# Kernel tuning notes

Measured on AMD Instinct MI355X. Metric: run time of the kernel, lower is better.

The kernel has to match this reference:

```python
import jax, jax.numpy as jnp
import numpy as np

VOCAB = 50257
EMB = 1024
HID = 1024
B, T = 8, 256


def setup_inputs() -> dict:
    key = jax.random.key(0)
    ks = jax.random.split(key, 6)
    s = 0.05  # small init scale for numerical sanity
    return {
        "x": jax.random.randint(ks[0], (B, T), 0, VOCAB, dtype=jnp.int64) if jax.config.jax_enable_x64 else jax.random.randint(ks[0], (B, T), 0, VOCAB, dtype=jnp.int32),
        "emb_W": jax.random.normal(ks[1], (VOCAB, EMB), dtype=jnp.float32) * s,
        "W_ih": jax.random.normal(ks[2], (4 * HID, EMB), dtype=jnp.float32) * s,
        "W_hh": jax.random.normal(ks[3], (4 * HID, HID), dtype=jnp.float32) * s,
        "b_ih": jax.random.normal(ks[4], (4 * HID,), dtype=jnp.float32) * s,
        "b_hh": jax.random.normal(ks[5], (4 * HID,), dtype=jnp.float32) * s,
        "dec_b": jnp.zeros((VOCAB,), dtype=jnp.float32),
    }


def _lstm(emb, W_ih, W_hh, b_ih, b_hh):
    # emb: [B, T, E]. Precompute input projections for all timesteps (one big GEMM).
    x_proj = jnp.einsum("bte,ge->btg", emb, W_ih) + (b_ih + b_hh)  # [B, T, 4H]
    h0 = jnp.zeros((emb.shape[0], HID), emb.dtype)
    c0 = jnp.zeros((emb.shape[0], HID), emb.dtype)

    def step(carry, xt):  # xt: [B, 4H]
        h, c = carry
        g = xt + h @ W_hh.T  # [B, 4H]
        i, f, gg, o = jnp.split(g, 4, axis=-1)  # PyTorch gate order i,f,g,o
        i = jax.nn.sigmoid(i)
        f = jax.nn.sigmoid(f)
        gg = jnp.tanh(gg)
        o = jax.nn.sigmoid(o)
        c_new = f * c + i * gg
        h_new = o * jnp.tanh(c_new)
        return (h_new, c_new), h_new

    (hT, cT), hs = jax.lax.scan(step, (h0, c0), jnp.swapaxes(x_proj, 0, 1))
    out = jnp.swapaxes(hs, 0, 1)  # [B, T, H], batch_first
    return out, (hT[None], cT[None])  # num_layers=1 leading dim


def reference(x, emb_W, W_ih, W_hh, b_ih, b_hh, dec_b):
    emb = emb_W[x]                                   # [B, T, E]
    out, hidden = _lstm(emb, W_ih, W_hh, b_ih, b_hh)  # [B, T, H]
    logits = jnp.einsum("bth,vh->btv", out, emb_W) + dec_b  # tied decoder
    logits = logits.reshape(-1, VOCAB)
    return jax.nn.log_softmax(logits, axis=1), hidden
```

## Files before the change

### kernel.cpp

```cpp
#include <hip/hip_runtime.h>

typedef float f32x4 __attribute__((ext_vector_type(4)));
typedef __bf16 bf16x8 __attribute__((ext_vector_type(8)));
typedef unsigned short u16;
typedef unsigned int u32;

#define VOCAB 50257
#define KDIM 1024
#define MROWS 2048
#define TSEQ 256
#define NBLK 64
#define LOGN ((size_t)MROWS * VOCAB)

__device__ __forceinline__ u16 f2bf(float f) {
    u32 u = __builtin_bit_cast(u32, f);
    u = (u + 0x7FFFu + ((u >> 16) & 1u)) >> 16;
    return (u16)u;
}

__device__ __forceinline__ float sigm(float x) { return 1.0f / (1.0f + __expf(-x)); }


__global__ void conv_bf16(const float4* __restrict__ in, ushort4* __restrict__ out, long n4) {
    long i = (long)blockIdx.x * blockDim.x + threadIdx.x;
    long stride = (long)gridDim.x * blockDim.x;
    for (; i < n4; i += stride) {
        float4 v = in[i];
        ushort4 o;
        o.x = f2bf(v.x); o.y = f2bf(v.y); o.z = f2bf(v.z); o.w = f2bf(v.w);
        out[i] = o;
    }
}

__global__ void bias_sum(const float* __restrict__ a, const float* __restrict__ b,
                         float* __restrict__ o) {
    int i = blockIdx.x * 256 + threadIdx.x;
    if (i < 4096) o[i] = a[i] + b[i];
}

__global__ __launch_bounds__(256) void gather_emb(const int* __restrict__ x,
                                                  const float* __restrict__ embW,
                                                  u16* __restrict__ out) {
    int m = blockIdx.x;
    int row = x[m];
    const float4* src = (const float4*)(embW + (size_t)row * KDIM);
    ushort4* dst = (ushort4*)(out + (size_t)m * KDIM);
    float4 v = src[threadIdx.x];
    ushort4 o;
    o.x = f2bf(v.x); o.y = f2bf(v.y); o.z = f2bf(v.z); o.w = f2bf(v.w);
    dst[threadIdx.x] = o;
}


#define BM 128
#define BN 128
#define BK 64

__device__ __forceinline__ void gl_lds16(const u16* g, const u16* l) {
    __builtin_amdgcn_global_load_lds(
        (const __attribute__((address_space(1))) u32*)g,
        (__attribute__((address_space(3))) u32*)l, 16, 0, 0);
}

__global__ __launch_bounds__(256, 2)
void gemm_bt(const u16* __restrict__ A, const u16* __restrict__ Bm,
             const float* __restrict__ bias, float* __restrict__ C,
             int N, int Nb, int K, int ldc)
{
    __shared__ __align__(16) u16 As[BM * BK];
    __shared__ __align__(16) u16 Bs[BN * BK];
    const int tid  = threadIdx.x;
    const int lane = tid & 63;
    const int wid  = tid >> 6;

    const int gx  = gridDim.x;
    const int nwg = gx * gridDim.y;
    const int lin = blockIdx.y * gx + blockIdx.x;
    const int qq = nwg >> 3, rr = nwg & 7;
    const int xcd = lin & 7, idx = lin >> 3;
    const int neu = (xcd < rr) ? (xcd * (qq + 1) + idx)
                               : (rr * (qq + 1) + (xcd - rr) * qq + idx);
    const int bm = neu % gx;
    const int bn = neu / gx;

    const int wr = wid >> 1, wc = wid & 1;

    const u16* gA[4]; const u16* gB[4];
    const u16* ldsA[4]; const u16* ldsB[4];
#pragma unroll
    for (int r = 0; r < 4; ++r) {
        int L = r * 256 + tid;
        int row = L >> 3, ps = L & 7;
        int ls = ps ^ (row & 7);
        gA[r] = A + (size_t)(bm * BM + row) * K + ls * 8;
        int brow = bn * BN + row; brow = brow < Nb ? brow : Nb - 1;
        gB[r] = Bm + (size_t)brow * K + ls * 8;
        ldsA[r] = As + (r * 256 + wid * 64) * 8;
        ldsB[r] = Bs + (r * 256 + wid * 64) * 8;
    }

    const int lrow = lane & 15, ksl = lane >> 4;
    int aoff[4][2], boff[4][2];
#pragma unroll
    for (int i = 0; i < 4; ++i)
#pragma unroll
        for (int ks = 0; ks < 2; ++ks) {
            int ar = wr * 64 + i * 16 + lrow;
            aoff[i][ks] = ar * BK + (((ks * 4 + ksl) ^ (ar & 7)) * 8);
            int br = wc * 64 + i * 16 + lrow;
            boff[i][ks] = br * BK + (((ks * 4 + ksl) ^ (br & 7)) * 8);
        }

    f32x4 acc[4][4] = {};
    for (int kt = 0; kt < K; kt += BK) {
#pragma unroll
        for (int r = 0; r < 4; ++r) gl_lds16(gA[r] + kt, ldsA[r]);
#pragma unroll
        for (int r = 0; r < 4; ++r) gl_lds16(gB[r] + kt, ldsB[r]);
        __syncthreads();
        bf16x8 af[4][2], bfb[4][2];
#pragma unroll
        for (int i = 0; i < 4; ++i)
#pragma unroll
            for (int ks = 0; ks < 2; ++ks) {
                af[i][ks]  = *(const bf16x8*)(As + aoff[i][ks]);
                bfb[i][ks] = *(const bf16x8*)(Bs + boff[i][ks]);
            }
#pragma unroll
        for (int ks = 0; ks < 2; ++ks)
#pragma unroll
            for (int mi = 0; mi < 4; ++mi)
#pragma unroll
                for (int ni = 0; ni < 4; ++ni)
                    acc[mi][ni] = __builtin_amdgcn_mfma_f32_16x16x32_bf16(
                        af[mi][ks], bfb[ni][ks], acc[mi][ni], 0, 0, 0);
        __syncthreads();
    }

    const int crl = lane >> 4, ccl = lane & 15;
    const int row0 = bm * BM + wr * 64, col0 = bn * BN + wc * 64;
#pragma unroll
    for (int ni = 0; ni < 4; ++ni) {
        int col = col0 + ni * 16 + ccl;
        if (col < N) {
            float bv = bias[col];
#pragma unroll
            for (int mi = 0; mi < 4; ++mi) {
                int row = row0 + mi * 16 + crl * 4;
                float* cp = C + (size_t)row * ldc + col;
#pragma unroll
                for (int r = 0; r < 4; ++r)
                    cp[(size_t)r * ldc] = acc[mi][ni][r] + bv;
            }
        }
    }
}


__global__ __launch_bounds__(256, 1)
void lstm_persist(const u16* __restrict__ Whh,
                  const float* __restrict__ xproj,
                  u16* __restrict__ hbuf2,
                  u16* __restrict__ hall,
                  float* __restrict__ outTail,
                  u32* __restrict__ flags)
{
    const int tid  = threadIdx.x;
    const int lane = tid & 63;
    const int wq   = tid >> 6;
    const int lrow = lane & 15, ksl = lane >> 4;
    const int bid  = blockIdx.x;
    const int colbase = bid * 16;

    bf16x8 Bf[32];
    {
        const u16* bp = Whh + (size_t)(wq * 1024 + colbase + lrow) * KDIM + ksl * 8;
#pragma unroll
        for (int kk = 0; kk < 32; ++kk)
            asm volatile("global_load_dwordx4 %0, %1, off"
                         : "=v"(Bf[kk]) : "v"(bp + kk * 32));
        asm volatile("s_waitcnt vmcnt(0)" ::: "memory");
        __builtin_amdgcn_sched_barrier(0);
    }

    __shared__ float S[4][8][16];

    const bool upd = tid < 128;
    const int b8 = tid >> 4, c16 = tid & 15;
    float creg = 0.f;
    float xp0 = 0.f, xp1 = 0.f, xp2 = 0.f, xp3 = 0.f;
    size_t xbase = 0;
    if (upd) {
        xbase = (size_t)b8 * TSEQ * 4096 + colbase + c16;
        xp0 = xproj[xbase];          xp1 = xproj[xbase + 1024];
        xp2 = xproj[xbase + 2048];   xp3 = xproj[xbase + 3072];
    }

    const u16* abase0 = hbuf2 + (ksl >> 1) * 256 + lrow * 16 + (ksl & 1) * 8;

    for (int t = 0; t < TSEQ; ++t) {
        const u16* ab = abase0 + (t & 1) * 16384;
        f32x4 ac0 = {}, ac1 = {}, ac2 = {}, ac3 = {};
        bf16x8 AB[2][4];
#pragma unroll
        for (int i = 0; i < 4; ++i)
            asm volatile("global_load_dwordx4 %0, %1, off sc0 sc1"
                         : "=v"(AB[0][i]) : "v"(ab + (size_t)i * 512));
#pragma unroll
        for (int i = 0; i < 4; ++i)
            asm volatile("global_load_dwordx4 %0, %1, off sc0 sc1"
                         : "=v"(AB[1][i]) : "v"(ab + (size_t)(4 + i) * 512));
#pragma unroll
        for (int g = 0; g < 8; ++g) {
            if (g < 7) asm volatile("s_waitcnt vmcnt(4)" ::: "memory");
            else       asm volatile("s_waitcnt vmcnt(0)" ::: "memory");
            __builtin_amdgcn_sched_barrier(0);
            ac0 = __builtin_amdgcn_mfma_f32_16x16x32_bf16(AB[g & 1][0], Bf[g * 4 + 0], ac0, 0, 0, 0);
            ac1 = __builtin_amdgcn_mfma_f32_16x16x32_bf16(AB[g & 1][1], Bf[g * 4 + 1], ac1, 0, 0, 0);
            ac2 = __builtin_amdgcn_mfma_f32_16x16x32_bf16(AB[g & 1][2], Bf[g * 4 + 2], ac2, 0, 0, 0);
            ac3 = __builtin_amdgcn_mfma_f32_16x16x32_bf16(AB[g & 1][3], Bf[g * 4 + 3], ac3, 0, 0, 0);
            if (g < 6) {
#pragma unroll
                for (int i = 0; i < 4; ++i)
                    asm volatile("global_load_dwordx4 %0, %1, off sc0 sc1"
                                 : "=v"(AB[g & 1][i])
                                 : "v"(ab + (size_t)((g + 2) * 4 + i) * 512));
            }
        }
        if (ksl < 2) {
#pragma unroll
            for (int r = 0; r < 4; ++r)
                S[wq][ksl * 4 + r][lrow] = ac0[r] + ac1[r] + ac2[r] + ac3[r];
        }
        __syncthreads();

        float hv = 0.f;
        u16 hb = 0;
        if (upd) {
            float gi = S[0][b8][c16] + xp0;
            float gf = S[1][b8][c16] + xp1;
            float gg = S[2][b8][c16] + xp2;
            float go = S[3][b8][c16] + xp3;
            float iv = sigm(gi), fv = sigm(gf), ov = sigm(go);
            float gv = tanhf(gg);
            creg = fv * creg + iv * gv;
            hv = ov * tanhf(creg);
            hb = f2bf(hv);
            int w0 = (int)hb;
            int w1 = __shfl_down(w0, 1);
            if (!(c16 & 1)) {
                u32 w = (u32)(u16)w0 | ((u32)(u16)w1 << 16);
                u32* dst = (u32*)hbuf2 + ((t + 1) & 1) * 8192 + bid * 128 + b8 * 8 + (c16 >> 1);
                __hip_atomic_store(dst, w, __ATOMIC_RELAXED, __HIP_MEMORY_SCOPE_AGENT);
            }
        }
        __syncthreads();
        if (tid == 0)
            __hip_atomic_store(flags + bid * 32, (u32)(t + 1),
                               __ATOMIC_RELAXED, __HIP_MEMORY_SCOPE_AGENT);
        if (upd) {
            hall[((size_t)b8 * TSEQ + t) * KDIM + colbase + c16] = hb;
            if (t == TSEQ - 1) {
                outTail[b8 * KDIM + colbase + c16] = hv;
                outTail[8192 + b8 * KDIM + colbase + c16] = creg;
            }
            int tn = (t + 1 < TSEQ) ? t + 1 : t;
            size_t xb = xbase + (size_t)tn * 4096;
            xp0 = xproj[xb];        xp1 = xproj[xb + 1024];
            xp2 = xproj[xb + 2048]; xp3 = xproj[xb + 3072];
        }
        if (tid < NBLK) {
            while (__hip_atomic_load(flags + tid * 32, __ATOMIC_RELAXED,
                                     __HIP_MEMORY_SCOPE_AGENT) < (u32)(t + 1))
                __builtin_amdgcn_s_sleep(1);
        }
        __syncthreads();
    }
}


__global__ __launch_bounds__(256)
void logsoftmax_rows(float* __restrict__ out) {
    const int m = blockIdx.x;
    float* row = out + (size_t)m * VOCAB;
    const int tid = threadIdx.x;
    __shared__ float smx[4], ssm[4], slse;

    const int head = (int)(((16 - ((uintptr_t)row & 15)) & 15) >> 2);
    const int nv = (VOCAB - head) >> 2;
    const int tail0 = head + nv * 4;
    const int ntail = VOCAB - tail0;
    const float4* rv = (const float4*)(row + head);

    float mx = -3.0e38f, s = 0.f;
    for (int i = tid; i < nv; i += 256) {
        float4 v = rv[i];
        float m4 = fmaxf(fmaxf(v.x, v.y), fmaxf(v.z, v.w));
        if (m4 > mx) { s *= __expf(mx - m4); mx = m4; }
        s += __expf(v.x - mx) + __expf(v.y - mx) + __expf(v.z - mx) + __expf(v.w - mx);
    }
    if (tid < head) {
        float v = row[tid];
        if (v > mx) { s *= __expf(mx - v); mx = v; }
        s += __expf(v - mx);
    }
    if (tid >= 64 && tid < 64 + ntail) {
        float v = row[tail0 + (tid - 64)];
        if (v > mx) { s *= __expf(mx - v); mx = v; }
        s += __expf(v - mx);
    }
#pragma unroll
    for (int off = 32; off > 0; off >>= 1) {
        float om = __shfl_xor(mx, off), os = __shfl_xor(s, off);
        float nm = fmaxf(mx, om);
        s = s * __expf(mx - nm) + os * __expf(om - nm);
        mx = nm;
    }
    if ((tid & 63) == 0) { smx[tid >> 6] = mx; ssm[tid >> 6] = s; }
    __syncthreads();
    if (tid == 0) {
        float M = fmaxf(fmaxf(smx[0], smx[1]), fmaxf(smx[2], smx[3]));
        float S4 = ssm[0] * __expf(smx[0] - M) + ssm[1] * __expf(smx[1] - M) +
                   ssm[2] * __expf(smx[2] - M) + ssm[3] * __expf(smx[3] - M);
        slse = M + __logf(S4);
    }
    __syncthreads();
    const float lse = slse;

    float4* wv = (float4*)(row + head);
    for (int i = tid; i < nv; i += 256) {
        float4 v = rv[i];
        v.x -= lse; v.y -= lse; v.z -= lse; v.w -= lse;
        wv[i] = v;
    }
    if (tid < head) row[tid] -= lse;
    if (tid >= 64 && tid < 64 + ntail) row[tail0 + (tid - 64)] -= lse;
}


extern "C" void kernel_launch(void* const* d_in, const int* in_sizes, int n_in,
                              void* d_out, int out_size, void* d_ws, size_t ws_size,
                              hipStream_t stream)
{
    const int*   x    = (const int*)d_in[0];
    const float* embW = (const float*)d_in[1];
    const float* Wih  = (const float*)d_in[2];
    const float* Whh  = (const float*)d_in[3];
    const float* bih  = (const float*)d_in[4];
    const float* bhh  = (const float*)d_in[5];
    const float* decb = (const float*)d_in[6];
    float* out = (float*)d_out;

    char* p = (char*)d_ws;
    auto carve = [&](size_t bytes) {
        char* q = p;
        p += (bytes + 255) & ~(size_t)255;
        return q;
    };
    u16*   embW_bf = (u16*)carve((size_t)VOCAB * KDIM * 2);
    u16*   Wih_bf  = (u16*)carve((size_t)4096 * KDIM * 2);
    u16*   Whh_bf  = (u16*)carve((size_t)4096 * KDIM * 2);
    u16*   emb_bf  = (u16*)carve((size_t)MROWS * KDIM * 2);
    float* xproj   = (float*)carve((size_t)MROWS * 4096 * 4);
    u16*   hall_bf = (u16*)carve((size_t)MROWS * KDIM * 2);
    u16*   hbuf2   = (u16*)carve((size_t)2 * 64 * 16 * 16 * 2);
    float* bsum    = (float*)carve((size_t)4096 * 4);
    u32*   flags   = (u32*)carve((size_t)NBLK * 32 * 4);

    hipMemsetAsync(hbuf2, 0, (size_t)2 * 64 * 16 * 16 * 2, stream);
    hipMemsetAsync(flags, 0, (size_t)NBLK * 32 * 4, stream);

    conv_bf16<<<1024, 256, 0, stream>>>((const float4*)Wih, (ushort4*)Wih_bf,
                                        (long)4096 * KDIM / 4);
    conv_bf16<<<1024, 256, 0, stream>>>((const float4*)Whh, (ushort4*)Whh_bf,
                                        (long)4096 * KDIM / 4);
    conv_bf16<<<2048, 256, 0, stream>>>((const float4*)embW, (ushort4*)embW_bf,
                                        (long)VOCAB * KDIM / 4);
    bias_sum<<<16, 256, 0, stream>>>(bih, bhh, bsum);
    gather_emb<<<MROWS, 256, 0, stream>>>(x, embW, emb_bf);

    {
        dim3 g(MROWS / BM, 4096 / BN);
        gemm_bt<<<g, 256, 0, stream>>>(emb_bf, Wih_bf, bsum, xproj, 4096, 4096, KDIM, 4096);
    }

    lstm_persist<<<NBLK, 256, 0, stream>>>(Whh_bf, xproj, hbuf2, hall_bf,
                                           out + LOGN, flags);

    {
        dim3 g(MROWS / BM, (VOCAB + BN - 1) / BN);
        gemm_bt<<<g, 256, 0, stream>>>(hall_bf, embW_bf, decb, out, VOCAB, VOCAB, KDIM, VOCAB);
    }

    logsoftmax_rows<<<MROWS, 256, 0, stream>>>(out);
}
```

Measured before the change: 1.408 ms.

## Replace LSTM grid barrier with data-polling and fuse softmax stats into decoder GEMM

Measured after the change: 1.566 ms. +11.2%, slower.

```diff
diff --git a/kernel.cpp b/kernel.cpp
--- a/kernel.cpp
+++ b/kernel.cpp
@@ -2,6 +2,7 @@
 
 typedef float f32x4 __attribute__((ext_vector_type(4)));
 typedef __bf16 bf16x8 __attribute__((ext_vector_type(8)));
+typedef unsigned int u32x4 __attribute__((ext_vector_type(4)));
 typedef unsigned short u16;
 typedef unsigned int u32;
 
@@ -10,6 +11,8 @@
 #define MROWS 2048
 #define TSEQ 256
 #define NBLK 64
+#define NTILE 393
+#define NT (NTILE * 2)
 #define LOGN ((size_t)MROWS * VOCAB)
 
 __device__ __forceinline__ u16 f2bf(float f) {
@@ -19,6 +22,13 @@
 }
 
 __device__ __forceinline__ float sigm(float x) { return 1.0f / (1.0f + __expf(-x)); }
+
+__device__ __forceinline__ u32 frag_min(bf16x8 v) {
+    u32x4 w = __builtin_bit_cast(u32x4, v);
+    u32 a = w.x < w.y ? w.x : w.y;
+    u32 b = w.z < w.w ? w.z : w.w;
+    return a < b ? a : b;
+}
 
 
 __global__ void conv_bf16(const float4* __restrict__ in, ushort4* __restrict__ out, long n4) {
@@ -51,6 +61,15 @@
     dst[threadIdx.x] = o;
 }
 
+__global__ void init_hseq(u32* __restrict__ hs) {
+    int i = blockIdx.x * 256 + threadIdx.x;
+    if (i < 257 * 8192) {
+        int s = i >> 13;
+        int row = (i >> 3) & 15;
+        hs[i] = (s == 0 || row >= 8) ? 0x00010001u : 0u;
+    }
+}
+
 
 #define BM 128
 #define BN 128
@@ -157,13 +176,135 @@
 }
 
 
+__global__ __launch_bounds__(256, 2)
+void gemm_dec(const u16* __restrict__ A, const u16* __restrict__ Bm,
+              const float* __restrict__ bias, float* __restrict__ C,
+              float* __restrict__ pmax, float* __restrict__ psum)
+{
+    const int N = VOCAB, Nb = VOCAB, K = KDIM, ldc = VOCAB;
+    __shared__ __align__(16) u16 As[BM * BK];
+    __shared__ __align__(16) u16 Bs[BN * BK];
+    const int tid  = threadIdx.x;
+    const int lane = tid & 63;
+    const int wid  = tid >> 6;
+
+    const int gx  = gridDim.x;
+    const int nwg = gx * gridDim.y;
+    const int lin = blockIdx.y * gx + blockIdx.x;
+    const int qq = nwg >> 3, rr = nwg & 7;
+    const int xcd = lin & 7, idx = lin >> 3;
+    const int neu = (xcd < rr) ? (xcd * (qq + 1) + idx)
+                               : (rr * (qq + 1) + (xcd - rr) * qq + idx);
+    const int bm = neu % gx;
+    const int bn = neu / gx;
+
+    const int wr = wid >> 1, wc = wid & 1;
+
+    const u16* gA[4]; const u16* gB[4];
+    const u16* ldsA[4]; const u16* ldsB[4];
+#pragma unroll
+    for (int r = 0; r < 4; ++r) {
+        int L = r * 256 + tid;
+        int row = L >> 3, ps = L & 7;
+        int ls = ps ^ (row & 7);
+        gA[r] = A + (size_t)(bm * BM + row) * K + ls * 8;
+        int brow = bn * BN + row; brow = brow < Nb ? brow : Nb - 1;
+        gB[r] = Bm + (size_t)brow * K + ls * 8;
+        ldsA[r] = As + (r * 256 + wid * 64) * 8;
+        ldsB[r] = Bs + (r * 256 + wid * 64) * 8;
+    }
+
+    const int lrow = lane & 15, ksl = lane >> 4;
+    int aoff[4][2], boff[4][2];
+#pragma unroll
+    for (int i = 0; i < 4; ++i)
+#pragma unroll
+        for (int ks = 0; ks < 2; ++ks) {
+            int ar = wr * 64 + i * 16 + lrow;
+            aoff[i][ks] = ar * BK + (((ks * 4 + ksl) ^ (ar & 7)) * 8);
+            int br = wc * 64 + i * 16 + lrow;
+            boff[i][ks] = br * BK + (((ks * 4 + ksl) ^ (br & 7)) * 8);
+        }
+
+    f32x4 acc[4][4] = {};
+    for (int kt = 0; kt < K; kt += BK) {
+#pragma unroll
+        for (int r = 0; r < 4; ++r) gl_lds16(gA[r] + kt, ldsA[r]);
+#pragma unroll
+        for (int r = 0; r < 4; ++r) gl_lds16(gB[r] + kt, ldsB[r]);
+        __syncthreads();
+        bf16x8 af[4][2], bfb[4][2];
+#pragma unroll
+        for (int i = 0; i < 4; ++i)
+#pragma unroll
+            for (int ks = 0; ks < 2; ++ks) {
+                af[i][ks]  = *(const bf16x8*)(As + aoff[i][ks]);
+                bfb[i][ks] = *(const bf16x8*)(Bs + boff[i][ks]);
+            }
+#pragma unroll
+        for (int ks = 0; ks < 2; ++ks)
+#pragma unroll
+            for (int mi = 0; mi < 4; ++mi)
+#pragma unroll
+                for (int ni = 0; ni < 4; ++ni)
+                    acc[mi][ni] = __builtin_amdgcn_mfma_f32_16x16x32_bf16(
+                        af[mi][ks], bfb[ni][ks], acc[mi][ni], 0, 0, 0);
+        __syncthreads();
+    }
+
+    const int crl = lane >> 4, ccl = lane & 15;
+    const int row0 = bm * BM + wr * 64, col0 = bn * BN + wc * 64;
+    float bve[4]; bool vld[4];
+#pragma unroll
+    for (int ni = 0; ni < 4; ++ni) {
+        int col = col0 + ni * 16 + ccl;
+        vld[ni] = col < N;
+        bve[ni] = vld[ni] ? bias[col] : 0.f;
+    }
+#pragma unroll
+    for (int ni = 0; ni < 4; ++ni) {
+        if (vld[ni]) {
+            int col = col0 + ni * 16 + ccl;
+#pragma unroll
+            for (int mi = 0; mi < 4; ++mi) {
+                int row = row0 + mi * 16 + crl * 4;
+                float* cp = C + (size_t)row * ldc + col;
+#pragma unroll
+                for (int r = 0; r < 4; ++r)
+                    cp[(size_t)r * ldc] = acc[mi][ni][r] + bve[ni];
+            }
+        }
+    }
+#pragma unroll
+    for (int mi = 0; mi < 4; ++mi)
+#pragma unroll
+        for (int r = 0; r < 4; ++r) {
+            int row = row0 + mi * 16 + crl * 4 + r;
+            float v0 = vld[0] ? acc[mi][0][r] + bve[0] : -3.0e38f;
+            float v1 = vld[1] ? acc[mi][1][r] + bve[1] : -3.0e38f;
+            float v2 = vld[2] ? acc[mi][2][r] + bve[2] : -3.0e38f;
+            float v3 = vld[3] ? acc[mi][3][r] + bve[3] : -3.0e38f;
+            float rmax = fmaxf(fmaxf(v0, v1), fmaxf(v2, v3));
+#pragma unroll
+            for (int m2 = 1; m2 < 16; m2 <<= 1) rmax = fmaxf(rmax, __shfl_xor(rmax, m2));
+            float rs = __expf(v0 - rmax) + __expf(v1 - rmax) +
+                       __expf(v2 - rmax) + __expf(v3 - rmax);
+#pragma unroll
+            for (int m2 = 1; m2 < 16; m2 <<= 1) rs += __shfl_xor(rs, m2);
+            if (ccl == 0) {
+                pmax[(size_t)row * NT + bn * 2 + wc] = rmax;
+                psum[(size_t)row * NT + bn * 2 + wc] = rs;
+            }
+        }
+}
+
+
 __global__ __launch_bounds__(256, 1)
 void lstm_persist(const u16* __restrict__ Whh,
                   const float* __restrict__ xproj,
-                  u16* __restrict__ hbuf2,
+                  u16* __restrict__ hseq,
                   u16* __restrict__ hall,
-                  float* __restrict__ outTail,
-                  u32* __restrict__ flags)
+                  float* __restrict__ outTail)
 {
     const int tid  = threadIdx.x;
     const int lane = tid & 63;
@@ -196,35 +337,49 @@
         xp2 = xproj[xbase + 2048];   xp3 = xproj[xbase + 3072];
     }
 
-    const u16* abase0 = hbuf2 + (ksl >> 1) * 256 + lrow * 16 + (ksl & 1) * 8;
+    const u16* abase0 = hseq + (ksl >> 1) * 256 + lrow * 16 + (ksl & 1) * 8;
 
     for (int t = 0; t < TSEQ; ++t) {
-        const u16* ab = abase0 + (t & 1) * 16384;
+        const u16* ab = abase0 + (size_t)t * 16384;
         f32x4 ac0 = {}, ac1 = {}, ac2 = {}, ac3 = {};
         bf16x8 AB[2][4];
 #pragma unroll
-        for (int i = 0; i < 4; ++i)
+        for (int i = 0; i < 8; ++i)
             asm volatile("global_load_dwordx4 %0, %1, off sc0 sc1"
-                         : "=v"(AB[0][i]) : "v"(ab + (size_t)i * 512));
-#pragma unroll
-        for (int i = 0; i < 4; ++i)
-            asm volatile("global_load_dwordx4 %0, %1, off sc0 sc1"
-                         : "=v"(AB[1][i]) : "v"(ab + (size_t)(4 + i) * 512));
+                         : "=v"(AB[(i >> 2) & 1][i & 3]) : "v"(ab + (size_t)i * 512));
 #pragma unroll
         for (int g = 0; g < 8; ++g) {
             if (g < 7) asm volatile("s_waitcnt vmcnt(4)" ::: "memory");
             else       asm volatile("s_waitcnt vmcnt(0)" ::: "memory");
             __builtin_amdgcn_sched_barrier(0);
-            ac0 = __builtin_amdgcn_mfma_f32_16x16x32_bf16(AB[g & 1][0], Bf[g * 4 + 0], ac0, 0, 0, 0);
-            ac1 = __builtin_amdgcn_mfma_f32_16x16x32_bf16(AB[g & 1][1], Bf[g * 4 + 1], ac1, 0, 0, 0);
-            ac2 = __builtin_amdgcn_mfma_f32_16x16x32_bf16(AB[g & 1][2], Bf[g * 4 + 2], ac2, 0, 0, 0);
-            ac3 = __builtin_amdgcn_mfma_f32_16x16x32_bf16(AB[g & 1][3], Bf[g * 4 + 3], ac3, 0, 0, 0);
-            if (g < 6) {
+            const int p = g & 1;
+            u32 m0 = frag_min(AB[p][0]), m1 = frag_min(AB[p][1]);
+            u32 m2 = frag_min(AB[p][2]), m3 = frag_min(AB[p][3]);
+            u32 mn = (m0 < m1 ? m0 : m1);
+            u32 mn2 = (m2 < m3 ? m2 : m3);
+            mn = mn < mn2 ? mn : mn2;
+            while (__builtin_expect(mn == 0u, 0)) {
 #pragma unroll
                 for (int i = 0; i < 4; ++i)
                     asm volatile("global_load_dwordx4 %0, %1, off sc0 sc1"
-                                 : "=v"(AB[g & 1][i])
-                                 : "v"(ab + (size_t)((g + 2) * 4 + i) * 512));
+                                 : "=v"(AB[p][i]) : "v"(ab + (size_t)(g * 4 + i) * 512));
+                asm volatile("s_waitcnt vmcnt(0)" ::: "memory");
+                __builtin_amdgcn_sched_barrier(0);
+                m0 = frag_min(AB[p][0]); m1 = frag_min(AB[p][1]);
+                m2 = frag_min(AB[p][2]); m3 = frag_min(AB[p][3]);
+                mn = (m0 < m1 ? m0 : m1);
+                mn2 = (m2 < m3 ? m2 : m3);
+                mn = mn < mn2 ? mn : mn2;
+            }
+            ac0 = __builtin_amdgcn_mfma_f32_16x16x32_bf16(AB[p][0], Bf[g * 4 + 0], ac0, 0, 0, 0);
+            ac1 = __builtin_amdgcn_mfma_f32_16x16x32_bf16(AB[p][1], Bf[g * 4 + 1], ac1, 0, 0, 0);
+            ac2 = __builtin_amdgcn_mfma_f32_16x16x32_bf16(AB[p][2], Bf[g * 4 + 2], ac2, 0, 0, 0);
+            ac3 = __builtin_amdgcn_mfma_f32_16x16x32_bf16(AB[p][3], Bf[g * 4 + 3], ac3, 0, 0, 0);
+            if (g < 6) {
+#pragma unroll
+                for (int i = 0; i < 4; ++i)
+                    asm volatile("global_load_dwordx4 %0, %1, off sc0 sc1"
+                                 : "=v"(AB[p][i]) : "v"(ab + (size_t)((g + 2) * 4 + i) * 512));
             }
         }
         if (ksl < 2) {
@@ -233,9 +388,6 @@
                 S[wq][ksl * 4 + r][lrow] = ac0[r] + ac1[r] + ac2[r] + ac3[r];
         }
         __syncthreads();
-
-        float hv = 0.f;
-        u16 hb = 0;
         if (upd) {
             float gi = S[0][b8][c16] + xp0;
             float gf = S[1][b8][c16] + xp1;
@@ -244,22 +396,16 @@
             float iv = sigm(gi), fv = sigm(gf), ov = sigm(go);
             float gv = tanhf(gg);
             creg = fv * creg + iv * gv;
-            hv = ov * tanhf(creg);
-            hb = f2bf(hv);
-            int w0 = (int)hb;
+            float hv = ov * tanhf(creg);
+            u16 hbx = f2bf(hv) | 1;
+            int w0 = (int)hbx;
             int w1 = __shfl_down(w0, 1);
             if (!(c16 & 1)) {
                 u32 w = (u32)(u16)w0 | ((u32)(u16)w1 << 16);
-                u32* dst = (u32*)hbuf2 + ((t + 1) & 1) * 8192 + bid * 128 + b8 * 8 + (c16 >> 1);
+                u32* dst = (u32*)hseq + (size_t)(t + 1) * 8192 + bid * 128 + b8 * 8 + (c16 >> 1);
                 __hip_atomic_store(dst, w, __ATOMIC_RELAXED, __HIP_MEMORY_SCOPE_AGENT);
             }
-        }
-        __syncthreads();
-        if (tid == 0)
-            __hip_atomic_store(flags + bid * 32, (u32)(t + 1),
-                               __ATOMIC_RELAXED, __HIP_MEMORY_SCOPE_AGENT);
-        if (upd) {
-            hall[((size_t)b8 * TSEQ + t) * KDIM + colbase + c16] = hb;
+            hall[((size_t)b8 * TSEQ + t) * KDIM + colbase + c16] = hbx;
             if (t == TSEQ - 1) {
                 outTail[b8 * KDIM + colbase + c16] = hv;
                 outTail[8192 + b8 * KDIM + colbase + c16] = creg;
@@ -269,45 +415,22 @@
             xp0 = xproj[xb];        xp1 = xproj[xb + 1024];
             xp2 = xproj[xb + 2048]; xp3 = xproj[xb + 3072];
         }
-        if (tid < NBLK) {
-            while (__hip_atomic_load(flags + tid * 32, __ATOMIC_RELAXED,
-                                     __HIP_MEMORY_SCOPE_AGENT) < (u32)(t + 1))
-                __builtin_amdgcn_s_sleep(1);
-        }
-        __syncthreads();
     }
 }
 
 
 __global__ __launch_bounds__(256)
-void logsoftmax_rows(float* __restrict__ out) {
+void merge_lse(const float* __restrict__ pmax, const float* __restrict__ psum,
+               float* __restrict__ lse) {
     const int m = blockIdx.x;
-    float* row = out + (size_t)m * VOCAB;
     const int tid = threadIdx.x;
-    __shared__ float smx[4], ssm[4], slse;
-
-    const int head = (int)(((16 - ((uintptr_t)row & 15)) & 15) >> 2);
-    const int nv = (VOCAB - head) >> 2;
-    const int tail0 = head + nv * 4;
-    const int ntail = VOCAB - tail0;
-    const float4* rv = (const float4*)(row + head);
-
+    __shared__ float smx[4], ssm[4];
     float mx = -3.0e38f, s = 0.f;
-    for (int i = tid; i < nv; i += 256) {
-        float4 v = rv[i];
-        float m4 = fmaxf(fmaxf(v.x, v.y), fmaxf(v.z, v.w));
-        if (m4 > mx) { s *= __expf(mx - m4); mx = m4; }
-        s += __expf(v.x - mx) + __expf(v.y - mx) + __expf(v.z - mx) + __expf(v.w - mx);
-    }
-    if (tid < head) {
-        float v = row[tid];
-        if (v > mx) { s *= __expf(mx - v); mx = v; }
-        s += __expf(v - mx);
-    }
-    if (tid >= 64 && tid < 64 + ntail) {
-        float v = row[tail0 + (tid - 64)];
-        if (v > mx) { s *= __expf(mx - v); mx = v; }
-        s += __expf(v - mx);
+    for (int i = tid; i < NT; i += 256) {
+        float pm = pmax[(size_t)m * NT + i];
+        float ps = psum[(size_t)m * NT + i];
+        if (pm > mx) { s *= __expf(mx - pm); mx = pm; }
+        s += ps * __expf(pm - mx);
     }
 #pragma unroll
     for (int off = 32; off > 0; off >>= 1) {
@@ -322,19 +445,28 @@
         float M = fmaxf(fmaxf(smx[0], smx[1]), fmaxf(smx[2], smx[3]));
         float S4 = ssm[0] * __expf(smx[0] - M) + ssm[1] * __expf(smx[1] - M) +
                    ssm[2] * __expf(smx[2] - M) + ssm[3] * __expf(smx[3] - M);
-        slse = M + __logf(S4);
-    }
-    __syncthreads();
-    const float lse = slse;
-
-    float4* wv = (float4*)(row + head);
+        lse[m] = M + __logf(S4);
+    }
+}
+
+__global__ __launch_bounds__(256)
+void final_sub(float* __restrict__ out, const float* __restrict__ lse) {
+    const int m = blockIdx.x;
+    float* row = out + (size_t)m * VOCAB;
+    const float L = lse[m];
+    const int tid = threadIdx.x;
+    const int head = (int)(((16 - ((uintptr_t)row & 15)) & 15) >> 2);
+    const int nv = (VOCAB - head) >> 2;
+    const int tail0 = head + nv * 4;
+    const int ntail = VOCAB - tail0;
+    float4* rv = (float4*)(row + head);
     for (int i = tid; i < nv; i += 256) {
         float4 v = rv[i];
-        v.x -= lse; v.y -= lse; v.z -= lse; v.w -= lse;
-        wv[i] = v;
-    }
-    if (tid < head) row[tid] -= lse;
-    if (tid >= 64 && tid < 64 + ntail) row[tail0 + (tid - 64)] -= lse;
+        v.x -= L; v.y -= L; v.z -= L; v.w -= L;
+        rv[i] = v;
+    }
+    if (tid < head) row[tid] -= L;
+    if (tid >= 64 && tid < 64 + ntail) row[tail0 + (tid - 64)] -= L;
 }
 
 
@@ -363,12 +495,13 @@
     u16*   emb_bf  = (u16*)carve((size_t)MROWS * KDIM * 2);
     float* xproj   = (float*)carve((size_t)MROWS * 4096 * 4);
     u16*   hall_bf = (u16*)carve((size_t)MROWS * KDIM * 2);
-    u16*   hbuf2   = (u16*)carve((size_t)2 * 64 * 16 * 16 * 2);
+    u16*   hseq    = (u16*)carve((size_t)(TSEQ + 1) * 16384 * 2);
+    float* pmax    = (float*)carve((size_t)MROWS * NT * 4);
+    float* psum    = (float*)carve((size_t)MROWS * NT * 4);
+    float* lse     = (float*)carve((size_t)MROWS * 4);
     float* bsum    = (float*)carve((size_t)4096 * 4);
-    u32*   flags   = (u32*)carve((size_t)NBLK * 32 * 4);
-
-    hipMemsetAsync(hbuf2, 0, (size_t)2 * 64 * 16 * 16 * 2, stream);
-    hipMemsetAsync(flags, 0, (size_t)NBLK * 32 * 4, stream);
+
+    init_hseq<<<(257 * 8192 + 255) / 256, 256, 0, stream>>>((u32*)hseq);
 
     conv_bf16<<<1024, 256, 0, stream>>>((const float4*)Wih, (ushort4*)Wih_bf,
                                         (long)4096 * KDIM / 4);
@@ -384,13 +517,13 @@
         gemm_bt<<<g, 256, 0, stream>>>(emb_bf, Wih_bf, bsum, xproj, 4096, 4096, KDIM, 4096);
     }
 
-    lstm_persist<<<NBLK, 256, 0, stream>>>(Whh_bf, xproj, hbuf2, hall_bf,
-                                           out + LOGN, flags);
+    lstm_persist<<<NBLK, 256, 0, stream>>>(Whh_bf, xproj, hseq, hall_bf, out + LOGN);
 
     {
-        dim3 g(MROWS / BM, (VOCAB + BN - 1) / BN);
-        gemm_bt<<<g, 256, 0, stream>>>(hall_bf, embW_bf, decb, out, VOCAB, VOCAB, KDIM, VOCAB);
-    }
-
-    logsoftmax_rows<<<MROWS, 256, 0, stream>>>(out);
-}
+        dim3 g(MROWS / BM, NTILE);
+        gemm_dec<<<g, 256, 0, stream>>>(hall_bf, embW_bf, decb, out, pmax, psum);
+    }
+
+    merge_lse<<<MROWS, 256, 0, stream>>>(pmax, psum, lse);
+    final_sub<<<MROWS, 256, 0, stream>>>(out, lse);
+}
```
